# Optimization experiments

Hardware: AMD Instinct MI355X
Metric: run time of the kernel (lower is better)

Reference implementation:

```python
import jax, jax.numpy as jnp
import numpy as np

N = 131072          # batch rows
D = 3               # number of feature dims (one small MLP per dim)
H = 128             # hidden width == inter_dim (hidden_sizes[0])


def setup_inputs() -> dict:
    key = jax.random.key(0)
    ks = jax.random.split(key, 12)
    x = jax.random.normal(ks[0], (N, D), dtype=jnp.float32)
    mask = jax.random.bernoulli(ks[1], 0.5, (N, D))
    s = 1.0 / np.sqrt(H)
    # Per-dim MLP: 1 -> 128 -> 128 -> 128 -> 128 (ReLU between layers).
    # Stack the 3 per-dim networks along a leading D axis.
    W0 = jax.random.normal(ks[2], (D, H), dtype=jnp.float32)            # in_dim = 1
    b0 = jax.random.normal(ks[3], (D, H), dtype=jnp.float32) * s
    W1 = jax.random.normal(ks[4], (D, H, H), dtype=jnp.float32) * s
    b1 = jax.random.normal(ks[5], (D, H), dtype=jnp.float32) * s
    W2 = jax.random.normal(ks[6], (D, H, H), dtype=jnp.float32) * s
    b2 = jax.random.normal(ks[7], (D, H), dtype=jnp.float32) * s
    W3 = jax.random.normal(ks[8], (D, H, H), dtype=jnp.float32) * s
    b3 = jax.random.normal(ks[9], (D, H), dtype=jnp.float32) * s
    return {"x": x, "mask": mask, "W0": W0, "b0": b0, "W1": W1, "b1": b1,
            "W2": W2, "b2": b2, "W3": W3, "b3": b3}


def reference(x, mask, W0, b0, W1, b1, W2, b2, W3, b3):
    # Vectorized equivalent of the per-dim gather -> MLP -> scatter loop:
    # unmasked rows contribute zeros (out is initialized to zeros and only
    # idx = where(mask[:, dim]) rows are written), so masked-multiply is exact.
    h = jax.nn.relu(x[:, :, None] * W0[None] + b0[None])          # [N, D, H]
    h = jax.nn.relu(jnp.einsum('ndh,dhk->ndk', h, W1) + b1[None])
    h = jax.nn.relu(jnp.einsum('ndh,dhk->ndk', h, W2) + b2[None])
    o = jnp.einsum('ndh,dhk->ndk', h, W3) + b3[None]              # [N, D, H]
    o = o * mask[:, :, None].astype(o.dtype)
    return jnp.sum(o, axis=1)                                     # [N, H]
```

## Files before the change

### kernel.cpp

```cpp
#include <hip/hip_runtime.h>
#include <hip/hip_bf16.h>
#include <cstdint>

#define HD 128

typedef __attribute__((ext_vector_type(8))) short short8;
typedef __attribute__((ext_vector_type(4))) float f32x4;
typedef __attribute__((ext_vector_type(4))) unsigned int u32x4;

static __device__ __forceinline__ short bf16_bits(float v) {
    __hip_bfloat16 h = __float2bfloat16(v);
    return __builtin_bit_cast(short, h);
}

__global__ __launch_bounds__(256) void precast_kernel(
    const float* __restrict__ W1, const float* __restrict__ W2,
    const float* __restrict__ W3, const unsigned char* __restrict__ mask,
    int n_mask, char* __restrict__ ws, int* __restrict__ mflag)
{
    if (blockIdx.x == 0 && blockIdx.y == 0) {
        __shared__ int any;
        if (threadIdx.x == 0) any = 0;
        __syncthreads();
        int limit = n_mask / 4;
        if (limit > 4096) limit = 4096;
        int local = 0;
        for (int k = threadIdx.x; k < limit; k += 256)
            local |= mask[4 * k + 1];
        if (local) atomicOr(&any, 1);
        __syncthreads();
        if (threadIdx.x == 0) *mflag = any;
    }
    const int s = blockIdx.x;
    const int d = s / 3, li = s % 3;
    const float* W = (li == 0 ? W1 : li == 1 ? W2 : W3) + d * HD * HD;
    const int t = threadIdx.x;
    const int p = blockIdx.y * 4 + (t >> 6);
    const int l = t & 63;
    const int kb = p >> 3, tm = p & 7;
    const int g = l >> 4;
    const int m = tm * 16 + (l & 15);
    const int jbase = 32 * kb + 4 * g;
    unsigned int pk[4];
    #pragma unroll
    for (int w = 0; w < 4; ++w) {
        const int j0 = jbase + (w >> 1) * 16 + (w & 1) * 2;
        const float a = W[j0 * HD + m];
        const float b = W[(j0 + 1) * HD + m];
        pk[w] = (unsigned short)bf16_bits(a) |
                ((unsigned)(unsigned short)bf16_bits(b) << 16);
    }
    *reinterpret_cast<u32x4*>(ws + s * 32768 + p * 1024 + l * 16) =
        u32x4{pk[0], pk[1], pk[2], pk[3]};
}

static __device__ __forceinline__ void stage_img(const char* __restrict__ src,
                                                 char* dst, int tid)
{
    #pragma unroll
    for (int it = 0; it < 8; ++it)
        __builtin_amdgcn_global_load_lds(
            (const __attribute__((address_space(1))) void*)(src + it * 4096 + tid * 16),
            (__attribute__((address_space(3))) void*)(dst + it * 4096 + tid * 16),
            16, 0, 0);
}

#define MFMA16(A, B, C) __builtin_amdgcn_mfma_f32_16x16x32_bf16(A, B, C, 0, 0, 0)

#define LAYER_MID(BSRC, BDST, BIAS, FOLDM)                                    \
  {                                                                           \
    _Pragma("unroll")                                                         \
    for (int pm = 0; pm < 4; ++pm) {                                          \
      f32x4 aA0, aA1, aB0, aB1;                                               \
      {                                                                       \
        const f32x4 bvA = *(const f32x4*)((BIAS) + (2 * pm) * 16 + g * 4);    \
        const f32x4 bvB = *(const f32x4*)((BIAS) + (2 * pm + 1) * 16 + g * 4);\
        aA0 = bvA; aA1 = bvA; aB0 = bvB; aB1 = bvB;                           \
      }                                                                       \
      _Pragma("unroll")                                                       \
      for (int kb = 0; kb < 4; ++kb) {                                        \
        const short8 a0 = *(const short8*)(wlds + (kb * 8 + 2 * pm) * 1024 + lofs);     \
        const short8 a1 = *(const short8*)(wlds + (kb * 8 + 2 * pm + 1) * 1024 + lofs); \
        aA0 = MFMA16(a0, BSRC[kb][0], aA0);                                   \
        aA1 = MFMA16(a0, BSRC[kb][1], aA1);                                   \
        aB0 = MFMA16(a1, BSRC[kb][0], aB0);                                   \
        aB1 = MFMA16(a1, BSRC[kb][1], aB1);                                   \
      }                                                                       \
      _Pragma("unroll")                                                       \
      for (int q = 0; q < 4; ++q) {                                           \
        float vA0 = fmaxf(aA0[q], 0.f), vA1 = fmaxf(aA1[q], 0.f);             \
        float vB0 = fmaxf(aB0[q], 0.f), vB1 = fmaxf(aB1[q], 0.f);             \
        if (FOLDM) { vA0 *= mkf0; vA1 *= mkf1; vB0 *= mkf0; vB1 *= mkf1; }    \
        BDST[pm][0][q]     = bf16_bits(vA0);                                  \
        BDST[pm][0][4 + q] = bf16_bits(vB0);                                  \
        BDST[pm][1][q]     = bf16_bits(vA1);                                  \
        BDST[pm][1][4 + q] = bf16_bits(vB1);                                  \
      }                                                                       \
    }                                                                         \
  }

#define LAYER_FIN(BSRC)                                                       \
  {                                                                           \
    _Pragma("unroll")                                                         \
    for (int pm = 0; pm < 4; ++pm) {                                          \
      _Pragma("unroll")                                                       \
      for (int kb = 0; kb < 4; ++kb) {                                        \
        const short8 a0 = *(const short8*)(wlds + (kb * 8 + 2 * pm) * 1024 + lofs);     \
        const short8 a1 = *(const short8*)(wlds + (kb * 8 + 2 * pm + 1) * 1024 + lofs); \
        acc3[2 * pm][0]     = MFMA16(a0, BSRC[kb][0], acc3[2 * pm][0]);       \
        acc3[2 * pm][1]     = MFMA16(a0, BSRC[kb][1], acc3[2 * pm][1]);       \
        acc3[2 * pm + 1][0] = MFMA16(a1, BSRC[kb][0], acc3[2 * pm + 1][0]);   \
        acc3[2 * pm + 1][1] = MFMA16(a1, BSRC[kb][1], acc3[2 * pm + 1][1]);   \
      }                                                                       \
    }                                                                         \
  }

__global__ __launch_bounds__(256, 3) void mlp_kernel(
    const float* __restrict__ x, const void* __restrict__ maskraw,
    const int* __restrict__ mflag,
    const float* __restrict__ W0, const float* __restrict__ b0,
    const float* __restrict__ b1, const float* __restrict__ b2,
    const float* __restrict__ b3, const char* __restrict__ wsWT,
    float* __restrict__ out)
{
    __shared__ char wlds[32768];
    const int tid  = threadIdx.x;
    const int wid  = tid >> 6;
    const int lane = tid & 63;
    const int r    = lane & 15;
    const int g    = lane >> 4;
    const int lofs = lane * 16;
    const int row0 = blockIdx.x * 128 + wid * 32;
    const bool bytewise = (*mflag != 0);
    const unsigned char* mask_b = (const unsigned char*)maskraw;
    const int*           mask_w = (const int*)maskraw;

    f32x4 acc3[8][2];
    #pragma unroll
    for (int tm = 0; tm < 8; ++tm)
        #pragma unroll
        for (int tc = 0; tc < 2; ++tc)
            acc3[tm][tc] = f32x4{0.f, 0.f, 0.f, 0.f};

    short8 bfA[4][2], bfB[4][2];

    stage_img(wsWT, wlds, tid);

    for (int d = 0; d < 3; ++d) {
        const int mi0 = (row0 + r) * 3 + d;
        const int mi1 = (row0 + 16 + r) * 3 + d;
        const float xv0 = x[mi0], xv1 = x[mi1];
        const float mkf0 = (bytewise ? (mask_b[mi0] != 0) : (mask_w[mi0] != 0)) ? 1.f : 0.f;
        const float mkf1 = (bytewise ? (mask_b[mi1] != 0) : (mask_w[mi1] != 0)) ? 1.f : 0.f;

        {
            const float* W0d = W0 + d * HD;
            const float* b0d = b0 + d * HD;
            #pragma unroll
            for (int kb = 0; kb < 4; ++kb) {
                const f32x4 w0a = *(const f32x4*)(W0d + kb * 32 + g * 4);
                const f32x4 w0b = *(const f32x4*)(W0d + kb * 32 + 16 + g * 4);
                const f32x4 bba = *(const f32x4*)(b0d + kb * 32 + g * 4);
                const f32x4 bbb = *(const f32x4*)(b0d + kb * 32 + 16 + g * 4);
                #pragma unroll
                for (int tc = 0; tc < 2; ++tc) {
                    const float xx = tc ? xv1 : xv0;
                    short8 f;
                    #pragma unroll
                    for (int q = 0; q < 4; ++q) {
                        f[q]     = bf16_bits(fmaxf(xx * w0a[q] + bba[q], 0.f));
                        f[4 + q] = bf16_bits(fmaxf(xx * w0b[q] + bbb[q], 0.f));
                    }
                    bfA[kb][tc] = f;
                }
            }
        }

        __syncthreads();
        LAYER_MID(bfA, bfB, b1 + d * HD, false);
        __syncthreads();
        stage_img(wsWT + (d * 3 + 1) * 32768, wlds, tid);

        __syncthreads();
        LAYER_MID(bfB, bfA, b2 + d * HD, true);
        __syncthreads();
        stage_img(wsWT + (d * 3 + 2) * 32768, wlds, tid);

        __syncthreads();
        LAYER_FIN(bfA);
        __syncthreads();
        if (d < 2) stage_img(wsWT + (d * 3 + 3) * 32768, wlds, tid);
    }

    #pragma unroll
    for (int tc = 0; tc < 2; ++tc) {
        const int row = row0 + tc * 16 + r;
        float mk[3];
        #pragma unroll
        for (int dd = 0; dd < 3; ++dd) {
            const int mi = row * 3 + dd;
            mk[dd] = (bytewise ? (mask_b[mi] != 0) : (mask_w[mi] != 0)) ? 1.f : 0.f;
        }
        float* orow = out + (long)row * HD;
        #pragma unroll
        for (int tm = 0; tm < 8; ++tm) {
            const f32x4 ba  = *(const f32x4*)(b3 + 0 * HD + tm * 16 + g * 4);
            const f32x4 bbv = *(const f32x4*)(b3 + 1 * HD + tm * 16 + g * 4);
            const f32x4 bc  = *(const f32x4*)(b3 + 2 * HD + tm * 16 + g * 4);
            f32x4 o = acc3[tm][tc];
            #pragma unroll
            for (int q = 0; q < 4; ++q)
                o[q] += mk[0] * ba[q] + mk[1] * bbv[q] + mk[2] * bc[q];
            *reinterpret_cast<f32x4*>(orow + tm * 16 + g * 4) = o;
        }
    }
}

extern "C" void kernel_launch(void* const* d_in, const int* in_sizes, int n_in,
                              void* d_out, int out_size, void* d_ws, size_t ws_size,
                              hipStream_t stream) {
    const float* x  = (const float*)d_in[0];
    const unsigned char* mask = (const unsigned char*)d_in[1];
    const float* W0 = (const float*)d_in[2];
    const float* b0 = (const float*)d_in[3];
    const float* W1 = (const float*)d_in[4];
    const float* b1 = (const float*)d_in[5];
    const float* W2 = (const float*)d_in[6];
    const float* b2 = (const float*)d_in[7];
    const float* W3 = (const float*)d_in[8];
    const float* b3 = (const float*)d_in[9];
    float* out = (float*)d_out;
    char* ws = (char*)d_ws;
    int* mflag = (int*)(ws + 9 * 32768);
    const int n_mask = in_sizes[1];

    hipLaunchKernelGGL(precast_kernel, dim3(9, 8), dim3(256), 0, stream,
                       W1, W2, W3, mask, n_mask, ws, mflag);
    hipLaunchKernelGGL(mlp_kernel, dim3(1024), dim3(256), 0, stream,
                       x, (const void*)mask, mflag, W0, b0, b1, b2, b3, ws, out);
}
```

Baseline: 148.4 us.

## Double-buffer half weight images in LDS and halve rows per block

Weight staging is split into two 16KB LDS halves so the next half loads while MFMAs run on the current one, replacing the previous stall-then-load pattern. Each wave now handles 16 rows instead of 32, with 2048 blocks and an occupancy target of 4, which cuts register use. Mask format detection and expansion move into a separate pre-kernel that writes float masks to the workspace, and a raw-mask fallback is kept. The cost is an extra kernel launch, more barriers, and half the reuse of each staged weight tile per load.

```diff
diff --git a/kernel.cpp b/kernel.cpp
--- a/kernel.cpp
+++ b/kernel.cpp
@@ -13,24 +13,38 @@
     return __builtin_bit_cast(short, h);
 }
 
+__global__ __launch_bounds__(256) void maskexp_kernel(
+    const unsigned char* __restrict__ mask, int n_mask,
+    float* __restrict__ mout)
+{
+    __shared__ int s_byte;
+    const int probe = mask[4 * threadIdx.x + 1];
+    if (threadIdx.x == 0) s_byte = 0;
+    __syncthreads();
+    if (probe) atomicOr(&s_byte, 1);
+    __syncthreads();
+    const bool bytewise = (s_byte != 0);
+    const int i0 = (blockIdx.x * 256 + threadIdx.x) * 4;
+    if (i0 >= n_mask) return;
+    float4 o;
+    if (bytewise) {
+        const unsigned int b = *reinterpret_cast<const unsigned int*>(mask + i0);
+        o.x = (b & 0xffu) ? 1.f : 0.f;
+        o.y = (b & 0xff00u) ? 1.f : 0.f;
+        o.z = (b & 0xff0000u) ? 1.f : 0.f;
+        o.w = (b & 0xff000000u) ? 1.f : 0.f;
+    } else {
+        const int4 v = *reinterpret_cast<const int4*>((const int*)mask + i0);
+        o.x = v.x ? 1.f : 0.f; o.y = v.y ? 1.f : 0.f;
+        o.z = v.z ? 1.f : 0.f; o.w = v.w ? 1.f : 0.f;
+    }
+    *reinterpret_cast<float4*>(mout + i0) = o;
+}
+
 __global__ __launch_bounds__(256) void precast_kernel(
     const float* __restrict__ W1, const float* __restrict__ W2,
-    const float* __restrict__ W3, const unsigned char* __restrict__ mask,
-    int n_mask, char* __restrict__ ws, int* __restrict__ mflag)
-{
-    if (blockIdx.x == 0 && blockIdx.y == 0) {
-        __shared__ int any;
-        if (threadIdx.x == 0) any = 0;
-        __syncthreads();
-        int limit = n_mask / 4;
-        if (limit > 4096) limit = 4096;
-        int local = 0;
-        for (int k = threadIdx.x; k < limit; k += 256)
-            local |= mask[4 * k + 1];
-        if (local) atomicOr(&any, 1);
-        __syncthreads();
-        if (threadIdx.x == 0) *mflag = any;
-    }
+    const float* __restrict__ W3, char* __restrict__ ws)
+{
     const int s = blockIdx.x;
     const int d = s / 3, li = s % 3;
     const float* W = (li == 0 ? W1 : li == 1 ? W2 : W3) + d * HD * HD;
@@ -54,11 +68,11 @@
         u32x4{pk[0], pk[1], pk[2], pk[3]};
 }
 
-static __device__ __forceinline__ void stage_img(const char* __restrict__ src,
-                                                 char* dst, int tid)
-{
-    #pragma unroll
-    for (int it = 0; it < 8; ++it)
+static __device__ __forceinline__ void stage_half(const char* __restrict__ src,
+                                                  char* dst, int tid)
+{
+    #pragma unroll
+    for (int it = 0; it < 4; ++it)
         __builtin_amdgcn_global_load_lds(
             (const __attribute__((address_space(1))) void*)(src + it * 4096 + tid * 16),
             (__attribute__((address_space(3))) void*)(dst + it * 4096 + tid * 16),
@@ -67,152 +81,165 @@
 
 #define MFMA16(A, B, C) __builtin_amdgcn_mfma_f32_16x16x32_bf16(A, B, C, 0, 0, 0)
 
-#define LAYER_MID(BSRC, BDST, BIAS, FOLDM)                                    \
-  {                                                                           \
-    _Pragma("unroll")                                                         \
-    for (int pm = 0; pm < 4; ++pm) {                                          \
-      f32x4 aA0, aA1, aB0, aB1;                                               \
-      {                                                                       \
-        const f32x4 bvA = *(const f32x4*)((BIAS) + (2 * pm) * 16 + g * 4);    \
-        const f32x4 bvB = *(const f32x4*)((BIAS) + (2 * pm + 1) * 16 + g * 4);\
-        aA0 = bvA; aA1 = bvA; aB0 = bvB; aB1 = bvB;                           \
+#define HALFL(BUF, BS, KB0)                                                   \
+  { _Pragma("unroll")                                                         \
+    for (int kk = 0; kk < 2; ++kk) {                                          \
+      const int kb = (KB0) + kk;                                              \
+      _Pragma("unroll")                                                       \
+      for (int tm = 0; tm < 8; ++tm) {                                        \
+        const short8 a = *(const short8*)((BUF) + (kk * 8 + tm) * 1024 + lofs);\
+        acct[tm] = MFMA16(a, BS[kb], acct[tm]);                               \
       }                                                                       \
+    } }
+
+#define HALFF(BUF, BS, KB0)                                                   \
+  { _Pragma("unroll")                                                         \
+    for (int kk = 0; kk < 2; ++kk) {                                          \
+      const int kb = (KB0) + kk;                                              \
       _Pragma("unroll")                                                       \
-      for (int kb = 0; kb < 4; ++kb) {                                        \
-        const short8 a0 = *(const short8*)(wlds + (kb * 8 + 2 * pm) * 1024 + lofs);     \
-        const short8 a1 = *(const short8*)(wlds + (kb * 8 + 2 * pm + 1) * 1024 + lofs); \
-        aA0 = MFMA16(a0, BSRC[kb][0], aA0);                                   \
-        aA1 = MFMA16(a0, BSRC[kb][1], aA1);                                   \
-        aB0 = MFMA16(a1, BSRC[kb][0], aB0);                                   \
-        aB1 = MFMA16(a1, BSRC[kb][1], aB1);                                   \
+      for (int tm = 0; tm < 8; ++tm) {                                        \
+        const short8 a = *(const short8*)((BUF) + (kk * 8 + tm) * 1024 + lofs);\
+        acc3[tm] = MFMA16(a, BS[kb], acc3[tm]);                               \
       }                                                                       \
+    } }
+
+#define BIASIN(B)                                                             \
+  { _Pragma("unroll")                                                         \
+    for (int tm = 0; tm < 8; ++tm)                                            \
+      acct[tm] = *(const f32x4*)((B) + tm * 16 + g * 4); }
+
+#define CONV(DST, DOMASK)                                                     \
+  { _Pragma("unroll")                                                         \
+    for (int kb = 0; kb < 4; ++kb) {                                          \
+      short8 f;                                                               \
       _Pragma("unroll")                                                       \
-      for (int q = 0; q < 4; ++q) {                                           \
-        float vA0 = fmaxf(aA0[q], 0.f), vA1 = fmaxf(aA1[q], 0.f);             \
-        float vB0 = fmaxf(aB0[q], 0.f), vB1 = fmaxf(aB1[q], 0.f);             \
-        if (FOLDM) { vA0 *= mkf0; vA1 *= mkf1; vB0 *= mkf0; vB1 *= mkf1; }    \
-        BDST[pm][0][q]     = bf16_bits(vA0);                                  \
-        BDST[pm][0][4 + q] = bf16_bits(vB0);                                  \
-        BDST[pm][1][q]     = bf16_bits(vA1);                                  \
-        BDST[pm][1][4 + q] = bf16_bits(vB1);                                  \
-      }                                                                       \
-    }                                                                         \
-  }
-
-#define LAYER_FIN(BSRC)                                                       \
-  {                                                                           \
-    _Pragma("unroll")                                                         \
-    for (int pm = 0; pm < 4; ++pm) {                                          \
-      _Pragma("unroll")                                                       \
-      for (int kb = 0; kb < 4; ++kb) {                                        \
-        const short8 a0 = *(const short8*)(wlds + (kb * 8 + 2 * pm) * 1024 + lofs);     \
-        const short8 a1 = *(const short8*)(wlds + (kb * 8 + 2 * pm + 1) * 1024 + lofs); \
-        acc3[2 * pm][0]     = MFMA16(a0, BSRC[kb][0], acc3[2 * pm][0]);       \
-        acc3[2 * pm][1]     = MFMA16(a0, BSRC[kb][1], acc3[2 * pm][1]);       \
-        acc3[2 * pm + 1][0] = MFMA16(a1, BSRC[kb][0], acc3[2 * pm + 1][0]);   \
-        acc3[2 * pm + 1][1] = MFMA16(a1, BSRC[kb][1], acc3[2 * pm + 1][1]);   \
-      }                                                                       \
-    }                                                                         \
-  }
-
-__global__ __launch_bounds__(256, 3) void mlp_kernel(
-    const float* __restrict__ x, const void* __restrict__ maskraw,
-    const int* __restrict__ mflag,
+      for (int hh = 0; hh < 2; ++hh)                                          \
+        _Pragma("unroll")                                                     \
+        for (int qq = 0; qq < 4; ++qq) {                                      \
+          float v = fmaxf(acct[2 * kb + hh][qq], 0.f);                        \
+          if (DOMASK) v *= mkf;                                               \
+          f[hh * 4 + qq] = bf16_bits(v);                                      \
+        }                                                                     \
+      DST[kb] = f;                                                            \
+    } }
+
+template<bool RAW>
+__global__ __launch_bounds__(256, 4) void mlp_kernel(
+    const float* __restrict__ x, const float* __restrict__ maskf,
+    const unsigned char* __restrict__ maskraw,
     const float* __restrict__ W0, const float* __restrict__ b0,
     const float* __restrict__ b1, const float* __restrict__ b2,
     const float* __restrict__ b3, const char* __restrict__ wsWT,
     float* __restrict__ out)
 {
-    __shared__ char wlds[32768];
+    __shared__ char buf0[16384];
+    __shared__ char buf1[16384];
+    __shared__ int s_byte;
+
     const int tid  = threadIdx.x;
     const int wid  = tid >> 6;
     const int lane = tid & 63;
     const int r    = lane & 15;
     const int g    = lane >> 4;
     const int lofs = lane * 16;
-    const int row0 = blockIdx.x * 128 + wid * 32;
-    const bool bytewise = (*mflag != 0);
-    const unsigned char* mask_b = (const unsigned char*)maskraw;
-    const int*           mask_w = (const int*)maskraw;
-
-    f32x4 acc3[8][2];
-    #pragma unroll
-    for (int tm = 0; tm < 8; ++tm)
-        #pragma unroll
-        for (int tc = 0; tc < 2; ++tc)
-            acc3[tm][tc] = f32x4{0.f, 0.f, 0.f, 0.f};
-
-    short8 bfA[4][2], bfB[4][2];
-
-    stage_img(wsWT, wlds, tid);
+    const int row  = blockIdx.x * 64 + wid * 16 + r;
+
+    stage_half(wsWT, buf0, tid);
+
+    bool bytewise = false;
+    if constexpr (RAW) {
+        const int probe = maskraw[4 * tid + 1];
+        if (tid == 0) s_byte = 0;
+        __syncthreads();
+        if (probe) atomicOr(&s_byte, 1);
+        __syncthreads();
+        bytewise = (s_byte != 0);
+    }
+
+    f32x4 acc3[8];
+    #pragma unroll
+    for (int tm = 0; tm < 8; ++tm) acc3[tm] = f32x4{0.f, 0.f, 0.f, 0.f};
+
+    short8 bfA[4], bfB[4];
+    f32x4  acct[8];
 
     for (int d = 0; d < 3; ++d) {
-        const int mi0 = (row0 + r) * 3 + d;
-        const int mi1 = (row0 + 16 + r) * 3 + d;
-        const float xv0 = x[mi0], xv1 = x[mi1];
-        const float mkf0 = (bytewise ? (mask_b[mi0] != 0) : (mask_w[mi0] != 0)) ? 1.f : 0.f;
-        const float mkf1 = (bytewise ? (mask_b[mi1] != 0) : (mask_w[mi1] != 0)) ? 1.f : 0.f;
+        const int mi = row * 3 + d;
+        const float xv = x[mi];
+        float mkf;
+        if constexpr (RAW)
+            mkf = (bytewise ? (maskraw[mi] != 0) : (((const int*)maskraw)[mi] != 0)) ? 1.f : 0.f;
+        else
+            mkf = maskf[mi];
 
         {
             const float* W0d = W0 + d * HD;
             const float* b0d = b0 + d * HD;
             #pragma unroll
             for (int kb = 0; kb < 4; ++kb) {
-                const f32x4 w0a = *(const f32x4*)(W0d + kb * 32 + g * 4);
-                const f32x4 w0b = *(const f32x4*)(W0d + kb * 32 + 16 + g * 4);
-                const f32x4 bba = *(const f32x4*)(b0d + kb * 32 + g * 4);
-                const f32x4 bbb = *(const f32x4*)(b0d + kb * 32 + 16 + g * 4);
+                short8 f;
                 #pragma unroll
-                for (int tc = 0; tc < 2; ++tc) {
-                    const float xx = tc ? xv1 : xv0;
-                    short8 f;
+                for (int hh = 0; hh < 2; ++hh) {
+                    const f32x4 w = *(const f32x4*)(W0d + kb * 32 + hh * 16 + g * 4);
+                    const f32x4 b = *(const f32x4*)(b0d + kb * 32 + hh * 16 + g * 4);
                     #pragma unroll
-                    for (int q = 0; q < 4; ++q) {
-                        f[q]     = bf16_bits(fmaxf(xx * w0a[q] + bba[q], 0.f));
-                        f[4 + q] = bf16_bits(fmaxf(xx * w0b[q] + bbb[q], 0.f));
-                    }
-                    bfA[kb][tc] = f;
+                    for (int qq = 0; qq < 4; ++qq)
+                        f[hh * 4 + qq] = bf16_bits(fmaxf(xv * w[qq] + b[qq], 0.f));
                 }
+                bfA[kb] = f;
             }
         }
 
-        __syncthreads();
-        LAYER_MID(bfA, bfB, b1 + d * HD, false);
-        __syncthreads();
-        stage_img(wsWT + (d * 3 + 1) * 32768, wlds, tid);
-
-        __syncthreads();
-        LAYER_MID(bfB, bfA, b2 + d * HD, true);
-        __syncthreads();
-        stage_img(wsWT + (d * 3 + 2) * 32768, wlds, tid);
-
-        __syncthreads();
-        LAYER_FIN(bfA);
-        __syncthreads();
-        if (d < 2) stage_img(wsWT + (d * 3 + 3) * 32768, wlds, tid);
-    }
-
-    #pragma unroll
-    for (int tc = 0; tc < 2; ++tc) {
-        const int row = row0 + tc * 16 + r;
-        float mk[3];
+        const char* i1 = wsWT + (size_t)(d * 3 + 0) * 32768;
+        const char* i2 = wsWT + (size_t)(d * 3 + 1) * 32768;
+        const char* i3 = wsWT + (size_t)(d * 3 + 2) * 32768;
+
+        __syncthreads();
+        stage_half(i1 + 16384, buf1, tid);
+        BIASIN(b1 + d * HD);
+        HALFL(buf0, bfA, 0);
+        __syncthreads();
+        stage_half(i2, buf0, tid);
+        HALFL(buf1, bfA, 2);
+        CONV(bfB, false);
+
+        __syncthreads();
+        stage_half(i2 + 16384, buf1, tid);
+        BIASIN(b2 + d * HD);
+        HALFL(buf0, bfB, 0);
+        __syncthreads();
+        stage_half(i3, buf0, tid);
+        HALFL(buf1, bfB, 2);
+        CONV(bfA, true);
+
+        __syncthreads();
+        stage_half(i3 + 16384, buf1, tid);
+        HALFF(buf0, bfA, 0);
+        __syncthreads();
+        if (d < 2) stage_half(wsWT + (size_t)(d * 3 + 3) * 32768, buf0, tid);
+        HALFF(buf1, bfA, 2);
+    }
+
+    float mk[3];
+    #pragma unroll
+    for (int dd = 0; dd < 3; ++dd) {
+        const int mi = row * 3 + dd;
+        if constexpr (RAW)
+            mk[dd] = (bytewise ? (maskraw[mi] != 0) : (((const int*)maskraw)[mi] != 0)) ? 1.f : 0.f;
+        else
+            mk[dd] = maskf[mi];
+    }
+    float* orow = out + (long)row * HD;
+    #pragma unroll
+    for (int tm = 0; tm < 8; ++tm) {
+        const f32x4 ba  = *(const f32x4*)(b3 + 0 * HD + tm * 16 + g * 4);
+        const f32x4 bbv = *(const f32x4*)(b3 + 1 * HD + tm * 16 + g * 4);
+        const f32x4 bc  = *(const f32x4*)(b3 + 2 * HD + tm * 16 + g * 4);
+        f32x4 o = acc3[tm];
         #pragma unroll
-        for (int dd = 0; dd < 3; ++dd) {
-            const int mi = row * 3 + dd;
-            mk[dd] = (bytewise ? (mask_b[mi] != 0) : (mask_w[mi] != 0)) ? 1.f : 0.f;
-        }
-        float* orow = out + (long)row * HD;
-        #pragma unroll
-        for (int tm = 0; tm < 8; ++tm) {
-            const f32x4 ba  = *(const f32x4*)(b3 + 0 * HD + tm * 16 + g * 4);
-            const f32x4 bbv = *(const f32x4*)(b3 + 1 * HD + tm * 16 + g * 4);
-            const f32x4 bc  = *(const f32x4*)(b3 + 2 * HD + tm * 16 + g * 4);
-            f32x4 o = acc3[tm][tc];
-            #pragma unroll
-            for (int q = 0; q < 4; ++q)
-                o[q] += mk[0] * ba[q] + mk[1] * bbv[q] + mk[2] * bc[q];
-            *reinterpret_cast<f32x4*>(orow + tm * 16 + g * 4) = o;
-        }
+        for (int qq = 0; qq < 4; ++qq)
+            o[qq] += mk[0] * ba[qq] + mk[1] * bbv[qq] + mk[2] * bc[qq];
+        *reinterpret_cast<f32x4*>(orow + tm * 16 + g * 4) = o;
     }
 }
 
@@ -231,11 +258,19 @@
     const float* b3 = (const float*)d_in[9];
     float* out = (float*)d_out;
     char* ws = (char*)d_ws;
-    int* mflag = (int*)(ws + 9 * 32768);
     const int n_mask = in_sizes[1];
+    float* maskf = (float*)(ws + 9 * 32768);
+    const size_t need = 9 * 32768 + (size_t)n_mask * 4;
 
     hipLaunchKernelGGL(precast_kernel, dim3(9, 8), dim3(256), 0, stream,
-                       W1, W2, W3, mask, n_mask, ws, mflag);
-    hipLaunchKernelGGL(mlp_kernel, dim3(1024), dim3(256), 0, stream,
-                       x, (const void*)mask, mflag, W0, b0, b1, b2, b3, ws, out);
-}
+                       W1, W2, W3, ws);
+    if (ws_size >= need) {
+        hipLaunchKernelGGL(maskexp_kernel, dim3((n_mask + 1023) / 1024), dim3(256),
+                           0, stream, mask, n_mask, maskf);
+        hipLaunchKernelGGL((mlp_kernel<false>), dim3(2048), dim3(256), 0, stream,
+                           x, maskf, mask, W0, b0, b1, b2, b3, ws, out);
+    } else {
+        hipLaunchKernelGGL((mlp_kernel<true>), dim3(2048), dim3(256), 0, stream,
+                           x, nullptr, mask, W0, b0, b1, b2, b3, ws, out);
+    }
+}
```

New measurement: 158.5 us. 1.07x slower.
